# Kernel optimization log

Hardware: AMD Instinct MI355X
Metric: run time of the kernel (lower is better)

Reference implementation:

```python
import jax, jax.numpy as jnp
import numpy as np
import math

N_VERT = 35709
N_FACE = 70789
BATCH = 32


def _normalize(x, axis=-1, eps=1e-12):
    n = jnp.linalg.norm(x, axis=axis, keepdims=True)
    return x / jnp.maximum(n, eps)


def setup_inputs() -> dict:
    key = jax.random.key(0)
    ks = jax.random.split(key, 9)
    coeff = jax.random.normal(ks[0], (BATCH, 277), jnp.float32)
    idBase = jax.random.normal(ks[1], (3 * N_VERT, 80), jnp.float32)
    exBase = jax.random.normal(ks[2], (3 * N_VERT, 64), jnp.float32)
    texBase = jax.random.normal(ks[3], (3 * N_VERT, 100), jnp.float32)
    meanshape = jax.random.normal(ks[4], (3 * N_VERT,), jnp.float32)
    meantex = jax.random.normal(ks[5], (3 * N_VERT,), jnp.float32)
    face_buf = jax.random.randint(ks[6], (N_FACE, 3), 0, N_VERT, jnp.int32)
    # point_buf may index the appended zero-normal row at position N_FACE (padding)
    point_buf = jax.random.randint(ks[7], (N_VERT, 8), 0, N_FACE + 1, jnp.int32)
    keypoints = jax.random.randint(ks[8], (68,), 0, N_VERT, jnp.int32)
    return dict(coeff=coeff, idBase=idBase, exBase=exBase, texBase=texBase,
                meanshape=meanshape, meantex=meantex, face_buf=face_buf,
                point_buf=point_buf, keypoints=keypoints)


def reference(coeff, idBase, exBase, texBase, meanshape, meantex,
              face_buf, point_buf, keypoints):
    B = coeff.shape[0]
    # ---- Split_coeff (canonical 80/64/100/3/27/3 layout) ----
    id_c = coeff[:, :80]
    ex_c = coeff[:, 80:144]
    tex_c = coeff[:, 144:244]
    angles = coeff[:, 244:247]
    gamma = coeff[:, 247:274]
    trans = coeff[:, 274:277]
    cam_scale = jnp.ones((B, 1), coeff.dtype)
    f_scale = jnp.ones((B, 1), coeff.dtype)

    # ---- Shape formation ----
    fs = (jnp.einsum('ij,aj->ai', idBase, id_c)
          + jnp.einsum('ij,aj->ai', exBase, ex_c)
          + meanshape[None, :])
    fs = fs.reshape(B, -1, 3)  # [B, N, 3]
    fs = fs - jnp.mean(meanshape.reshape(-1, 3), axis=0)[None, None, :]

    # ---- Texture formation ----
    tex = (jnp.einsum('ij,aj->ai', texBase, tex_c) + meantex[None, :]).reshape(B, -1, 3)

    # ---- Rotation matrix (Rz @ Ry @ Rx, then transpose) ----
    cx, sx = jnp.cos(angles[:, 0]), jnp.sin(angles[:, 0])
    cy, sy = jnp.cos(angles[:, 1]), jnp.sin(angles[:, 1])
    cz, sz = jnp.cos(angles[:, 2]), jnp.sin(angles[:, 2])
    o, z = jnp.ones_like(cx), jnp.zeros_like(cx)
    Rx = jnp.stack([o, z, z, z, cx, -sx, z, sx, cx], -1).reshape(B, 3, 3)
    Ry = jnp.stack([cy, z, sy, z, o, z, -sy, z, cy], -1).reshape(B, 3, 3)
    Rz = jnp.stack([cz, -sz, z, sz, cz, z, z, z, o], -1).reshape(B, 3, 3)
    rot = jnp.swapaxes(jnp.matmul(jnp.matmul(Rz, Ry), Rx), 1, 2)  # [B,3,3]

    # ---- Compute_norm: gather face verts, cross, aggregate to vertices ----
    v1 = fs[:, face_buf[:, 0], :]  # [B, F, 3]
    v2 = fs[:, face_buf[:, 1], :]
    v3 = fs[:, face_buf[:, 2], :]
    face_norm = _normalize(jnp.cross(v1 - v2, v2 - v3), axis=2)  # [B, F, 3]
    face_norm = jnp.concatenate(
        [face_norm, jnp.zeros((B, 1, 3), face_norm.dtype)], axis=1)  # pad row
    v_norm = _normalize(jnp.sum(face_norm[:, point_buf, :], axis=2), axis=2)  # [B,N,3]

    norm_r = jnp.matmul(v_norm, rot)

    # ---- Rigid transform + landmarks ----
    fst = jnp.matmul(fs, rot) + trans[:, None, :]
    lm = fst[:, keypoints, :]  # [B, 68, 3]

    # ---- Projection block (applied to landmarks) ----
    focal = 1015.0 * f_scale  # [B,1]
    camera_pos = jnp.array([0.0, 0.0, 10.0], coeff.dtype) * cam_scale[:, :, None]  # [B,1,3]
    reverse_z = jnp.diag(jnp.array([1.0, 1.0, -1.0], coeff.dtype))
    z1 = jnp.zeros((B, 1), coeff.dtype)
    z2 = jnp.zeros((B, 2), coeff.dtype)
    o1 = jnp.ones((B, 1), coeff.dtype)
    p_matrix = jnp.concatenate(
        [focal, z1, 112.0 * o1, z1, focal, 112.0 * o1, z2, o1], axis=1).reshape(B, 3, 3)
    lm_cam = jnp.matmul(lm, reverse_z[None]) + camera_pos
    aug = jnp.matmul(lm_cam, jnp.swapaxes(p_matrix, 1, 2))
    landmark_p = aug[..., :2] / aug[..., 2:3]

    # ---- SH illumination ----
    init_lit = jnp.array([0.8, 0, 0, 0, 0, 0, 0, 0, 0], coeff.dtype)
    g = gamma.reshape(B, 3, 9) + init_lit[None, None, :]
    pi = math.pi
    a0, a1, a2 = pi, 2 * pi / math.sqrt(3.0), 2 * pi / math.sqrt(8.0)
    c0 = 1.0 / math.sqrt(4 * pi)
    c1 = math.sqrt(3.0) / math.sqrt(4 * pi)
    c2 = 3 * math.sqrt(5.0) / math.sqrt(12 * pi)
    nx, ny, nz = norm_r[..., 0], norm_r[..., 1], norm_r[..., 2]
    Y = jnp.stack([
        a0 * c0 * jnp.ones_like(nx),
        -a1 * c1 * ny,
        a1 * c1 * nz,
        -a1 * c1 * nx,
        a2 * c2 * nx * ny,
        -a2 * c2 * ny * nz,
        a2 * c2 * 0.5 / math.sqrt(3.0) * (3 * nz * nz - 1),
        -a2 * c2 * nx * nz,
        a2 * c2 * 0.5 * (nx * nx - ny * ny),
    ], axis=-1)  # [B, N, 9]
    lighting = jnp.einsum('bnk,bck->bnc', Y, g)  # [B, N, 3]
    face_color = tex * lighting

    return face_color, landmark_p, fst
```

## Files before the change

### kernel.cpp

```cpp
#include <hip/hip_runtime.h>

#define N_VERT 35709
#define N_FACE 70789
#define NB 32
#define M3 (3*N_VERT)

#define WS_FS4X  ((size_t)0)
#define WS_FN4X  (WS_FS4X + (size_t)N_VERT*128)
#define WS_CPAD  (WS_FN4X + (size_t)(N_FACE+1)*128)
#define WS_ROT   (WS_CPAD + (size_t)NB*256)
#define WS_TRE   (WS_ROT + (size_t)NB*9)
#define WS_G     (WS_TRE + (size_t)NB*3)
#define WS_MEAN  (WS_G + (size_t)NB*27)

#define FC_OFF   ((size_t)0)
#define LM_OFF   ((size_t)NB*M3)
#define FST_OFF  (LM_OFF + (size_t)NB*68*2)

#define A0C0 0.88622692545275801f
#define A1C1 1.77245385090551603f
#define A2C2 2.42703239430f
#define Y6C  0.70062393935f
#define Y8C  1.21351619715f

__global__ void __launch_bounds__(256) face3d_stageA1(
    const float* __restrict__ ms, float* __restrict__ ws) {
  float s0=0.f, s1=0.f, s2=0.f;
  for (int v = blockIdx.x*256 + threadIdx.x; v < N_VERT; v += gridDim.x*256) {
    s0 += ms[3*v+0]; s1 += ms[3*v+1]; s2 += ms[3*v+2];
  }
  #pragma unroll
  for (int off = 32; off > 0; off >>= 1) {
    s0 += __shfl_down(s0, off);
    s1 += __shfl_down(s1, off);
    s2 += __shfl_down(s2, off);
  }
  if ((threadIdx.x & 63) == 0) {
    atomicAdd(&ws[WS_MEAN+0], s0);
    atomicAdd(&ws[WS_MEAN+1], s1);
    atomicAdd(&ws[WS_MEAN+2], s2);
  }
}

__global__ void __launch_bounds__(256) face3d_stageA2(
    const float* __restrict__ coeff, float* __restrict__ ws) {
  int t = threadIdx.x;
  float m0 = ws[WS_MEAN+0]*(1.0f/N_VERT);
  float m1 = ws[WS_MEAN+1]*(1.0f/N_VERT);
  float m2 = ws[WS_MEAN+2]*(1.0f/N_VERT);
  float4* cp4 = (float4*)(ws + WS_CPAD);
  for (int idx = t; idx < 64*32; idx += 256) {
    int s4 = idx >> 5, b = idx & 31;
    int k = 4*s4;
    float4 v;
    v.x = (k < 244) ? coeff[b*277 + k + 0] : 0.f;
    v.y = (k < 244) ? coeff[b*277 + k + 1] : 0.f;
    v.z = (k < 244) ? coeff[b*277 + k + 2] : 0.f;
    v.w = (k < 244) ? coeff[b*277 + k + 3] : 0.f;
    cp4[idx] = v;
  }
  for (int idx = t; idx < NB*27; idx += 256) {
    int b = idx / 27, k = idx - b*27;
    ws[WS_G + idx] = coeff[b*277 + 247 + k] + (((k % 9) == 0) ? 0.8f : 0.0f);
  }
  if (t < NB) {
    int b = t;
    float ax = coeff[b*277+244], ay = coeff[b*277+245], az = coeff[b*277+246];
    float cx=cosf(ax), sx=sinf(ax);
    float cy=cosf(ay), sy=sinf(ay);
    float cz=cosf(az), sz=sinf(az);
    float T00=cz*cy, T01=-sz, T02=cz*sy;
    float T10=sz*cy, T11=cz,  T12=sz*sy;
    float T20=-sy,   T21=0.f, T22=cy;
    float R[3][3];
    R[0][0]=T00; R[0][1]=T01*cx+T02*sx; R[0][2]=-T01*sx+T02*cx;
    R[1][0]=T10; R[1][1]=T11*cx+T12*sx; R[1][2]=-T11*sx+T12*cx;
    R[2][0]=T20; R[2][1]=T21*cx+T22*sx; R[2][2]=-T21*sx+T22*cx;
    float rot[3][3];
    #pragma unroll
    for (int c=0;c<3;c++)
      #pragma unroll
      for (int j=0;j<3;j++)
        rot[c][j] = R[j][c];
    #pragma unroll
    for (int c=0;c<3;c++)
      #pragma unroll
      for (int j=0;j<3;j++)
        ws[WS_ROT + b*9 + c*3 + j] = rot[c][j];
    #pragma unroll
    for (int j=0;j<3;j++)
      ws[WS_TRE + b*3 + j] = coeff[b*277+274+j]
        - (m0*rot[0][j] + m1*rot[1][j] + m2*rot[2][j]);
  }
}


template<int NK4, int SOFF>
__device__ __forceinline__ void gemm1(const float4* __restrict__ A,
                                      const float4* __restrict__ Wl,
                                      float* __restrict__ acc) {
  float4 p0 = A[0];
  float4 p1 = (NK4 > 1) ? A[1] : p0;
  #pragma unroll 1
  for (int s = 0; s < NK4; ++s) {
    float4 a = p0;
    p0 = p1;
    if (s + 2 < NK4) p1 = A[s+2];
    const float4* __restrict__ Ws = Wl + (size_t)(SOFF + s)*32;
    #pragma unroll
    for (int b = 0; b < NB; ++b) {
      float4 w = Ws[b];
      acc[b] = fmaf(a.w, w.w, fmaf(a.z, w.z, fmaf(a.y, w.y, fmaf(a.x, w.x, acc[b]))));
    }
  }
}

__global__ void __launch_bounds__(128) face3d_stageB(
    const float* __restrict__ idB, const float* __restrict__ exB,
    const float* __restrict__ texB, const float* __restrict__ meanshape,
    const float* __restrict__ meantex, const float* __restrict__ cpadT,
    float* __restrict__ fs4x, float* __restrict__ texOut) {
  __shared__ float4 Wl[36*32];
  int t = threadIdx.x;
  int bid = blockIdx.x;
  int isTex = bid & 1;
  int r = (bid >> 1)*128 + t;

  const float4* __restrict__ cp4 = (const float4*)cpadT;
  if (!isTex) {
    #pragma unroll
    for (int i = 0; i < 9; ++i) Wl[t + 128*i] = cp4[t + 128*i];
  } else {
    for (int i = t; i < 25*32; i += 128) Wl[i] = cp4[36*32 + i];
  }
  __syncthreads();
  if (r >= M3) return;

  float acc[NB];
  #pragma unroll
  for (int b = 0; b < NB; ++b) acc[b] = 0.f;

  if (!isTex) {
    gemm1<20, 0 >((const float4*)idB + (size_t)r*20, Wl, acc);
    gemm1<16, 20>((const float4*)exB + (size_t)r*16, Wl, acc);
    float msv = meanshape[r];
    int v = r/3, c = r - 3*v;
    float* dst = fs4x + (size_t)v*128 + c;
    #pragma unroll
    for (int b = 0; b < NB; ++b) dst[b*4] = acc[b] + msv;
  } else {
    gemm1<25, 0 >((const float4*)texB + (size_t)r*25, Wl, acc);
    float mtv = meantex[r];
    #pragma unroll
    for (int b = 0; b < NB; ++b) texOut[(size_t)b*M3 + r] = acc[b] + mtv;
  }
}

__global__ void __launch_bounds__(256) face3d_stageC(
    const int* __restrict__ face_buf, const float* __restrict__ fs4x,
    float* __restrict__ fn4x) {
  int t = threadIdx.x;
  int b = t & 31, fi = t >> 5;
  int f = blockIdx.x*8 + fi;
  if (f > N_FACE) return;
  float4* o = (float4*)(fn4x + ((size_t)f*32 + b)*4);
  if (f == N_FACE) { *o = make_float4(0.f,0.f,0.f,0.f); return; }
  int i0 = face_buf[f*3+0];
  int i1 = face_buf[f*3+1];
  int i2 = face_buf[f*3+2];
  float4 p1 = *(const float4*)(fs4x + ((size_t)i0*32 + b)*4);
  float4 p2 = *(const float4*)(fs4x + ((size_t)i1*32 + b)*4);
  float4 p3 = *(const float4*)(fs4x + ((size_t)i2*32 + b)*4);
  float e1x = p1.x-p2.x, e1y = p1.y-p2.y, e1z = p1.z-p2.z;
  float e2x = p2.x-p3.x, e2y = p2.y-p3.y, e2z = p2.z-p3.z;
  float nx = e1y*e2z - e1z*e2y;
  float ny = e1z*e2x - e1x*e2z;
  float nz = e1x*e2y - e1y*e2x;
  float inv = 1.0f / fmaxf(sqrtf(nx*nx + ny*ny + nz*nz), 1e-12f);
  *o = make_float4(nx*inv, ny*inv, nz*inv, 0.f);
}

__global__ void __launch_bounds__(256) face3d_stageD(
    const int* __restrict__ point_buf, const int* __restrict__ keypoints,
    const float* __restrict__ fs4x, const float* __restrict__ fn4x,
    const float* __restrict__ rotAll, const float* __restrict__ treAll,
    const float* __restrict__ gAll, float* __restrict__ out) {
  const int mainBlocks = (N_VERT + 7)/8;
  int bid = blockIdx.x;
  int t = threadIdx.x;
  if (bid < mainBlocks) {
    __shared__ float rotL[NB*9];
    __shared__ float treL[NB*3];
    __shared__ float gL[NB*27];
    __shared__ float fstL[NB*33];
    __shared__ float LL[NB*33];
    if (t < NB*9)  rotL[t] = rotAll[t];
    if (t < NB*3)  treL[t] = treAll[t];
    for (int i = t; i < NB*27; i += 256) gL[i] = gAll[i];
    __syncthreads();
    int b = t & 31, vi = t >> 5;
    int v0 = bid*8;
    int v = v0 + vi;
    if (v < N_VERT) {
      const int4 pb0 = *(const int4*)(point_buf + (size_t)v*8);
      const int4 pb1 = *(const int4*)(point_buf + (size_t)v*8 + 4);
      float4 g0 = *(const float4*)(fn4x + ((size_t)pb0.x*32 + b)*4);
      float4 g1 = *(const float4*)(fn4x + ((size_t)pb0.y*32 + b)*4);
      float4 g2 = *(const float4*)(fn4x + ((size_t)pb0.z*32 + b)*4);
      float4 g3 = *(const float4*)(fn4x + ((size_t)pb0.w*32 + b)*4);
      float4 g4 = *(const float4*)(fn4x + ((size_t)pb1.x*32 + b)*4);
      float4 g5 = *(const float4*)(fn4x + ((size_t)pb1.y*32 + b)*4);
      float4 g6 = *(const float4*)(fn4x + ((size_t)pb1.z*32 + b)*4);
      float4 g7 = *(const float4*)(fn4x + ((size_t)pb1.w*32 + b)*4);
      float sx = ((g0.x+g1.x)+(g2.x+g3.x)) + ((g4.x+g5.x)+(g6.x+g7.x));
      float sy = ((g0.y+g1.y)+(g2.y+g3.y)) + ((g4.y+g5.y)+(g6.y+g7.y));
      float sz = ((g0.z+g1.z)+(g2.z+g3.z)) + ((g4.z+g5.z)+(g6.z+g7.z));
      float inv = 1.0f / fmaxf(sqrtf(sx*sx + sy*sy + sz*sz), 1e-12f);
      float n0 = sx*inv, n1 = sy*inv, n2 = sz*inv;
      const float* rot = rotL + b*9;
      float r00=rot[0], r01=rot[1], r02=rot[2];
      float r10=rot[3], r11=rot[4], r12=rot[5];
      float r20=rot[6], r21=rot[7], r22=rot[8];
      float nx = n0*r00 + n1*r10 + n2*r20;
      float ny = n0*r01 + n1*r11 + n2*r21;
      float nz = n0*r02 + n1*r12 + n2*r22;
      float Y1 = -A1C1*ny;
      float Y2 =  A1C1*nz;
      float Y3 = -A1C1*nx;
      float Y4 =  A2C2*nx*ny;
      float Y5 = -A2C2*ny*nz;
      float Y6 =  Y6C*(3.f*nz*nz - 1.f);
      float Y7 = -A2C2*nx*nz;
      float Y8 =  Y8C*(nx*nx - ny*ny);
      const float* g = gL + b*27;
      #pragma unroll
      for (int c = 0; c < 3; ++c) {
        const float* gc = g + c*9;
        float Lc = A0C0*gc[0] + Y1*gc[1] + Y2*gc[2] + Y3*gc[3] + Y4*gc[4]
                 + Y5*gc[5] + Y6*gc[6] + Y7*gc[7] + Y8*gc[8];
        LL[b*33 + vi*4 + c] = Lc;
      }
      float4 fsv = *(const float4*)(fs4x + ((size_t)v*32 + b)*4);
      const float* tre = treL + b*3;
      fstL[b*33 + vi*4 + 0] = fsv.x*r00 + fsv.y*r10 + fsv.z*r20 + tre[0];
      fstL[b*33 + vi*4 + 1] = fsv.x*r01 + fsv.y*r11 + fsv.z*r21 + tre[1];
      fstL[b*33 + vi*4 + 2] = fsv.x*r02 + fsv.y*r12 + fsv.z*r22 + tre[2];
    }
    __syncthreads();
    int b2 = t >> 3, w = t & 7;
    if (v0 + w < N_VERT) {
      size_t obase = (size_t)b2*M3 + (size_t)(v0 + w)*3;
      float f0 = fstL[b2*33 + w*4 + 0];
      float f1 = fstL[b2*33 + w*4 + 1];
      float f2 = fstL[b2*33 + w*4 + 2];
      out[FST_OFF + obase + 0] = f0;
      out[FST_OFF + obase + 1] = f1;
      out[FST_OFF + obase + 2] = f2;
      float l0 = LL[b2*33 + w*4 + 0];
      float l1 = LL[b2*33 + w*4 + 1];
      float l2 = LL[b2*33 + w*4 + 2];
      float t0 = out[FC_OFF + obase + 0];
      float t1 = out[FC_OFF + obase + 1];
      float t2 = out[FC_OFF + obase + 2];
      out[FC_OFF + obase + 0] = t0*l0;
      out[FC_OFF + obase + 1] = t1*l1;
      out[FC_OFF + obase + 2] = t2*l2;
    }
  } else {
    int idx = (bid - mainBlocks)*256 + t;
    if (idx >= NB*68) return;
    int b = idx & 31, j = idx >> 5;
    int kp = keypoints[j];
    const float* rot = rotAll + b*9;
    const float* tre = treAll + b*3;
    float4 fsv = *(const float4*)(fs4x + ((size_t)kp*32 + b)*4);
    float o0 = fsv.x*rot[0] + fsv.y*rot[3] + fsv.z*rot[6] + tre[0];
    float o1 = fsv.x*rot[1] + fsv.y*rot[4] + fsv.z*rot[7] + tre[1];
    float o2 = fsv.x*rot[2] + fsv.y*rot[5] + fsv.z*rot[8] + tre[2];
    float zc = 10.0f - o2;
    float axv = 1015.0f*o0 + 112.0f*zc;
    float ayv = 1015.0f*o1 + 112.0f*zc;
    out[LM_OFF + (size_t)b*136 + (size_t)j*2 + 0] = axv/zc;
    out[LM_OFF + (size_t)b*136 + (size_t)j*2 + 1] = ayv/zc;
  }
}

extern "C" void kernel_launch(void* const* d_in, const int* in_sizes, int n_in,
                              void* d_out, int out_size, void* d_ws, size_t ws_size,
                              hipStream_t stream) {
  const float* coeff     = (const float*)d_in[0];
  const float* idB       = (const float*)d_in[1];
  const float* exB       = (const float*)d_in[2];
  const float* texB      = (const float*)d_in[3];
  const float* meanshape = (const float*)d_in[4];
  const float* meantex   = (const float*)d_in[5];
  const int*   face_buf  = (const int*)d_in[6];
  const int*   point_buf = (const int*)d_in[7];
  const int*   keypoints = (const int*)d_in[8];
  float* out = (float*)d_out;
  float* ws  = (float*)d_ws;

  hipMemsetAsync((char*)d_ws + WS_MEAN*sizeof(float), 0, 3*sizeof(float), stream);

  hipLaunchKernelGGL(face3d_stageA1, dim3(56), dim3(256), 0, stream, meanshape, ws);
  hipLaunchKernelGGL(face3d_stageA2, dim3(1), dim3(256), 0, stream, coeff, ws);

  int gridB = 2 * ((M3 + 127)/128);
  hipLaunchKernelGGL(face3d_stageB, dim3(gridB), dim3(128), 0, stream,
                     idB, exB, texB, meanshape, meantex,
                     ws + WS_CPAD, ws + WS_FS4X, out + FC_OFF);

  int gridC = (N_FACE + 1 + 7)/8;
  hipLaunchKernelGGL(face3d_stageC, dim3(gridC), dim3(256), 0, stream,
                     face_buf, ws + WS_FS4X, ws + WS_FN4X);

  int mainBlocks = (N_VERT + 7)/8;
  int lmBlocks   = (NB*68 + 255)/256;
  hipLaunchKernelGGL(face3d_stageD, dim3(mainBlocks + lmBlocks), dim3(256), 0, stream,
                     point_buf, keypoints, ws + WS_FS4X, ws + WS_FN4X,
                     ws + WS_ROT, ws + WS_TRE, ws + WS_G, out);
}
```

Before: 279.2 us.

## Stage basis rows through LDS with async global_load_lds double buffering

Replaces the per-thread strided float4 loads of basis rows in the GEMM stage with wave-cooperative global_load_lds copies into double-buffered LDS tiles. Each wave loads contiguous 16-byte chunks covering 64 rows, so global accesses are coalesced instead of row-strided, and the next tile is prefetched while the current one is computed, gated by explicit vmcnt waits. The cost is more LDS per block, which may lower occupancy, and reliance on hand-written waitcnt counts. Out-of-range rows are clamped instead of returning early.

```diff
diff --git a/kernel.cpp b/kernel.cpp
--- a/kernel.cpp
+++ b/kernel.cpp
@@ -95,23 +95,64 @@
 }
 
 
-template<int NK4, int SOFF>
-__device__ __forceinline__ void gemm1(const float4* __restrict__ A,
-                                      const float4* __restrict__ Wl,
-                                      float* __restrict__ acc) {
-  float4 p0 = A[0];
-  float4 p1 = (NK4 > 1) ? A[1] : p0;
-  #pragma unroll 1
-  for (int s = 0; s < NK4; ++s) {
-    float4 a = p0;
-    p0 = p1;
-    if (s + 2 < NK4) p1 = A[s+2];
-    const float4* __restrict__ Ws = Wl + (size_t)(SOFF + s)*32;
+__device__ __forceinline__ void gload16(const void* g, void* l) {
+  __builtin_amdgcn_global_load_lds((const __attribute__((address_space(1))) void*)g,
+                                   (__attribute__((address_space(3))) void*)l, 16, 0, 0);
+}
+
+#define WAITVM0() do { asm volatile("s_waitcnt vmcnt(0)" ::: "memory"); \
+                       __builtin_amdgcn_sched_barrier(0); } while (0)
+#define WAITVM4() do { asm volatile("s_waitcnt vmcnt(4)" ::: "memory"); \
+                       __builtin_amdgcn_sched_barrier(0); } while (0)
+#define WAITVM5() do { asm volatile("s_waitcnt vmcnt(5)" ::: "memory"); \
+                       __builtin_amdgcn_sched_barrier(0); } while (0)
+
+template<int K4, int TK4>
+__device__ __forceinline__ void stageTile(const float4* __restrict__ A, int r0w, int gk4,
+                                          int lane, float4* __restrict__ buf) {
+  #pragma unroll
+  for (int p = 0; p < TK4; ++p) {
+    int j = p*64 + lane;
+    int rl = j / TK4;
+    int sl = j - rl*TK4;
+    int row = r0w + rl; row = (row < M3) ? row : (M3-1);
+    gload16(A + (size_t)row*K4 + gk4 + sl, buf + j);
+  }
+}
+
+template<int TK4>
+__device__ __forceinline__ void compTile(const float4* __restrict__ Wl, int soff,
+                                         const float4* __restrict__ buf,
+                                         int lane, float* __restrict__ acc) {
+  #pragma unroll
+  for (int s = 0; s < TK4; ++s) {
+    float4 a = buf[lane*TK4 + s];
+    const float4* __restrict__ Ws = Wl + (size_t)(soff + s)*32;
     #pragma unroll
     for (int b = 0; b < NB; ++b) {
       float4 w = Ws[b];
       acc[b] = fmaf(a.w, w.w, fmaf(a.z, w.z, fmaf(a.y, w.y, fmaf(a.x, w.x, acc[b]))));
     }
+  }
+}
+
+template<int K4, int TK4, int NT, int SOFF>
+__device__ __forceinline__ void phase(const float4* __restrict__ A, int r0w,
+                                      const float4* __restrict__ Wl,
+                                      float4* __restrict__ buf0, float4* __restrict__ buf1,
+                                      int lane, float* __restrict__ acc) {
+  stageTile<K4, TK4>(A, r0w, 0, lane, buf0);
+  #pragma unroll 1
+  for (int tau = 0; tau < NT; ++tau) {
+    float4* cur = (tau & 1) ? buf1 : buf0;
+    float4* nxt = (tau & 1) ? buf0 : buf1;
+    if (tau + 1 < NT) {
+      stageTile<K4, TK4>(A, r0w, (tau+1)*TK4, lane, nxt);
+      if constexpr (TK4 == 5) WAITVM5(); else WAITVM4();
+    } else {
+      WAITVM0();
+    }
+    compTile<TK4>(Wl, SOFF + tau*TK4, cur, lane, acc);
   }
 }
 
@@ -120,11 +161,17 @@
     const float* __restrict__ texB, const float* __restrict__ meanshape,
     const float* __restrict__ meantex, const float* __restrict__ cpadT,
     float* __restrict__ fs4x, float* __restrict__ texOut) {
-  __shared__ float4 Wl[36*32];
+  __shared__ float4 lds[1152 + 4*320];
   int t = threadIdx.x;
   int bid = blockIdx.x;
   int isTex = bid & 1;
-  int r = (bid >> 1)*128 + t;
+  int lane = t & 63, wid = t >> 6;
+  int r0w = (bid >> 1)*128 + wid*64;
+  int r = r0w + lane;
+
+  float4* Wl = lds;
+  float4* buf0 = lds + 1152 + wid*640;
+  float4* buf1 = buf0 + 320;
 
   const float4* __restrict__ cp4 = (const float4*)cpadT;
   if (!isTex) {
@@ -134,25 +181,28 @@
     for (int i = t; i < 25*32; i += 128) Wl[i] = cp4[36*32 + i];
   }
   __syncthreads();
-  if (r >= M3) return;
 
   float acc[NB];
   #pragma unroll
   for (int b = 0; b < NB; ++b) acc[b] = 0.f;
 
   if (!isTex) {
-    gemm1<20, 0 >((const float4*)idB + (size_t)r*20, Wl, acc);
-    gemm1<16, 20>((const float4*)exB + (size_t)r*16, Wl, acc);
-    float msv = meanshape[r];
-    int v = r/3, c = r - 3*v;
-    float* dst = fs4x + (size_t)v*128 + c;
-    #pragma unroll
-    for (int b = 0; b < NB; ++b) dst[b*4] = acc[b] + msv;
+    phase<20, 5, 4, 0 >((const float4*)idB, r0w, Wl, buf0, buf1, lane, acc);
+    phase<16, 4, 4, 20>((const float4*)exB, r0w, Wl, buf0, buf1, lane, acc);
+    if (r < M3) {
+      float msv = meanshape[r];
+      int v = r/3, c = r - 3*v;
+      float* dst = fs4x + (size_t)v*128 + c;
+      #pragma unroll
+      for (int b = 0; b < NB; ++b) dst[b*4] = acc[b] + msv;
+    }
   } else {
-    gemm1<25, 0 >((const float4*)texB + (size_t)r*25, Wl, acc);
-    float mtv = meantex[r];
-    #pragma unroll
-    for (int b = 0; b < NB; ++b) texOut[(size_t)b*M3 + r] = acc[b] + mtv;
+    phase<25, 5, 5, 0 >((const float4*)texB, r0w, Wl, buf0, buf1, lane, acc);
+    if (r < M3) {
+      float mtv = meantex[r];
+      #pragma unroll
+      for (int b = 0; b < NB; ++b) texOut[(size_t)b*M3 + r] = acc[b] + mtv;
+    }
   }
 }
 
```

New measurement: 277.8 us. About the same (-0.5%).
